# Performance work log

Measured on AMD Instinct MI355X. Metric: run time of the kernel, lower is better.

Reference implementation:

```python
import jax, jax.numpy as jnp
from jax import lax
import numpy as np


def setup_inputs() -> dict:
    key = jax.random.key(0)
    kx, kw = jax.random.split(key)
    # Binary {0,1} activations: the module's int8-cast/XOR/AND trick is only
    # meaningful XNOR-popcount math for binary inputs.
    x = jax.random.randint(kx, (32, 256, 58, 58), 0, 2).astype(jnp.float32)
    weight = jax.random.normal(kw, (256, 256, 3, 3), dtype=jnp.float32)
    return {"x": x, "weight": weight}


def reference(x, weight):
    # XNORConv2d.forward, stride=1, padding=0 (forward never pads).
    B, C, H, W = x.shape
    O, _, kh, kw = weight.shape
    n = C * H * W  # note: alpha normalizes by INPUT size, as in the source
    N = kh * kw

    # alpha = sum_{c,kh,kw} |w| / n, one scalar per output filter  -> (O,)
    alpha = jnp.sum(jnp.abs(weight), axis=(1, 2, 3)) / n

    # Binarized weights: sign(w) >= 0 -> {0,1}
    bw = (weight >= 0).astype(x.dtype)

    dn = lax.conv_dimension_numbers(x.shape, weight.shape, ("NCHW", "OIHW", "NCHW"))
    conv = lambda a, f: lax.conv_general_dilated(
        a, f, window_strides=(1, 1), padding="VALID", dimension_numbers=dn
    )

    # XNOR match count per (b, o, y, x): S = #(p==f) over c,kh,kw
    #   = conv(p, f) + conv(1-p, 1-f)
    S = conv(x, bw) + conv(1.0 - x, 1.0 - bw)  # (B, O, H', W')

    # popcount per channel = 2*s_c - N; summed over channels -> 2*S - C*N
    res = 2.0 * S - jnp.asarray(C * N, dtype=x.dtype)

    return alpha[None, :, None, None] * res
```

## Files before the change

### kernel.cpp

```cpp
#include <hip/hip_runtime.h>
#include <stdint.h>


#define BATCH 32
#define C_IN 256
#define OCH 256
#define HIN 58
#define WIN2 58
#define HOUT 56
#define WOUT 56
#define TAPS 9
#define WWORDS 8
#define HWIN (HIN * WIN2)
#define HWOUT (HOUT * WOUT)
#define NPOS (BATCH * HWIN)

#define AP 144
#define NAPOS 232

typedef int   i32x4  __attribute__((ext_vector_type(4)));
typedef int   i32x16 __attribute__((ext_vector_type(16)));
typedef float f32x4  __attribute__((ext_vector_type(4)));

#define MFMA(acc, va, vb) \
    asm volatile("v_mfma_i32_32x32x32_i8 %0, %1, %2, %0" : "+v"(acc) : "v"(va), "v"(vb))

__global__ __launch_bounds__(256) void pack_x_kernel(
    const float* __restrict__ x, uint32_t* __restrict__ xp)
{
    int t = blockIdx.x * 256 + threadIdx.x;
    int p  = t >> 2;
    int wp = t & 3;
    int b = p / HWIN;
    int r = p - b * HWIN;
    const float* xb = x + ((size_t)(b * C_IN + wp * 64)) * HWIN + r;
    uint32_t m0 = 0u, m1 = 0u;
    #pragma unroll
    for (int j = 0; j < 32; ++j) {
        float v0 = xb[(size_t)j * HWIN];
        float v1 = xb[(size_t)(j + 32) * HWIN];
        m0 |= (v0 > 0.5f ? 1u : 0u) << j;
        m1 |= (v1 > 0.5f ? 1u : 0u) << j;
    }
    *(uint2*)(xp + (size_t)p * WWORDS + wp * 2) = make_uint2(m0, m1);
}

__global__ __launch_bounds__(256) void pack_w8_kernel(
    const float* __restrict__ wt, char* __restrict__ wq8s, float* __restrict__ sA)
{
    int o = blockIdx.x;
    int c = threadIdx.x;
    const float* wb = wt + ((size_t)o * C_IN + c) * TAPS;
    float s = 0.f;
    char sg[TAPS];
    #pragma unroll
    for (int t = 0; t < TAPS; ++t) {
        float v = wb[t];
        s += fabsf(v);
        sg[t] = (v >= 0.0f) ? (char)1 : (char)-1;
    }
    int kh = c >> 7;
    int kb = (c >> 5) & 3;
    int e  = (c >> 4) & 1;
    int j  = c & 15;
    #pragma unroll
    for (int t = 0; t < TAPS; ++t) {
        int st = kh * 36 + t * 4 + kb;
        wq8s[(size_t)((st * 2 + e) * 256 + o) * 16 + j] = sg[t];
    }

    __shared__ float red[256];
    red[c] = s;
    __syncthreads();
    for (int off = 128; off > 0; off >>= 1) {
        if (c < off) red[c] += red[c + off];
        __syncthreads();
    }
    if (c == 0) sA[o] = red[0] / (float)(C_IN * HWIN);
}

__global__ __launch_bounds__(512)
void xnor_mfma_kernel(
    const uint32_t* __restrict__ xp, const char* __restrict__ wq8s,
    const float* __restrict__ sA, float* __restrict__ out)
{
    __shared__ __attribute__((aligned(16))) char lds[36864];
    char* Alds = lds;
    float* Cbuf = (float*)lds;

    int blk = blockIdx.x;
    int b   = blk / 28;
    int rp  = blk - b * 28;
    int oy0 = rp * 2;
    int tid  = threadIdx.x;
    int wv   = tid >> 6;
    int lane = tid & 63;
    int l31  = lane & 31;
    int e    = lane >> 5;
    int mgrp = wv & 1;
    int ngrp = wv >> 1;

    int baseA[2];
    #pragma unroll
    for (int mi = 0; mi < 2; ++mi) {
        int p = (mgrp * 2 + mi) * 32 + l31;
        int r = (p * 586) >> 15;
        int c = p - 56 * r;
        baseA[mi] = (r * 58 + c) * AP + e * 16;
    }
    const char* pb = wq8s + ((size_t)e * 256 + (size_t)(ngrp * 64 + l31)) * 16;
    float al0 = sA[ngrp * 64 + l31];
    float al1 = sA[ngrp * 64 + 32 + l31];

    i32x16 acc00 = {0}, acc01 = {0}, acc10 = {0}, acc11 = {0};
    asm volatile("" : "+v"(acc00), "+v"(acc01), "+v"(acc10), "+v"(acc11));
    asm volatile("s_nop 7\n\ts_nop 7");

#define STAGE_A(KH)                                                        \
    {                                                                      \
        _Pragma("unroll")                                                  \
        for (int ir = 0; ir < 4; ++ir) {                                   \
            if (tid < 464) {                                               \
                int iw = tid >> 3, c16 = tid & 7;                          \
                uint32_t wvx = xp[((size_t)(b * HIN + oy0 + ir) * WIN2 + iw) * WWORDS \
                                  + (KH) * 4 + (c16 >> 1)];                \
                uint32_t bits = (c16 & 1) ? (wvx >> 16) : (wvx & 0xFFFFu); \
                i32x4 v;                                                   \
                _Pragma("unroll")                                          \
                for (int d = 0; d < 4; ++d) {                              \
                    uint32_t n  = (bits >> (4 * d)) & 0xFu;                \
                    uint32_t sp = (n * 0x204081u) & 0x01010101u;           \
                    v[d] = (int)~(sp * 0xFEu);                             \
                }                                                          \
                *(i32x4*)(Alds + (ir * 58 + iw) * AP + c16 * 16) = v;      \
            }                                                              \
        }                                                                  \
    }

    STAGE_A(0);

    i32x4 rb0[3], rb1[3];
    #pragma unroll
    for (int q = 0; q < 3; ++q) {
        rb0[q] = *(const i32x4*)(pb + (size_t)q * 8192);
        rb1[q] = *(const i32x4*)(pb + (size_t)q * 8192 + 512);
    }
    __syncthreads();

    #pragma unroll
    for (int s = 0; s < 72; ++s) {
        if (s == 36) {
            __syncthreads();
            STAGE_A(1);
            __syncthreads();
        }
        const int kh  = s / 36;
        const int tap = (s - kh * 36) >> 2;
        const int kb  = s & 3;
        const int dy  = tap / 3, dx = tap - dy * 3;
        const int ka  = (dy * 58 + dx) * AP + kb * 32;

        i32x4 a0 = *(const i32x4*)(Alds + baseA[0] + ka);
        i32x4 a1 = *(const i32x4*)(Alds + baseA[1] + ka);
        i32x4 b0 = rb0[s % 3];
        i32x4 b1 = rb1[s % 3];
        MFMA(acc00, a0, b0);
        MFMA(acc01, a0, b1);
        MFMA(acc10, a1, b0);
        MFMA(acc11, a1, b1);

        const int s3 = (s + 3 > 71) ? 71 : s + 3;
        rb0[s % 3] = *(const i32x4*)(pb + (size_t)s3 * 8192);
        rb1[s % 3] = *(const i32x4*)(pb + (size_t)s3 * 8192 + 512);
    }

    asm volatile("s_nop 7\n\ts_nop 7");

    size_t ob = ((size_t)b * OCH) * HWOUT + (size_t)oy0 * WOUT;
    #pragma unroll
    for (int q = 0; q < 4; ++q) {
        __syncthreads();
        if (mgrp == (q >> 1)) {
            const int mi = q & 1;
            #pragma unroll
            for (int ni = 0; ni < 2; ++ni) {
                float al = ni ? al1 : al0;
                int o = ngrp * 64 + ni * 32 + l31;
                i32x16 A;
                if (mi == 0 && ni == 0) A = acc00;
                else if (mi == 0)       A = acc01;
                else if (ni == 0)       A = acc10;
                else                    A = acc11;
                #pragma unroll
                for (int g = 0; g < 4; ++g) {
                    f32x4 vv;
                    vv[0] = al * (float)A[4 * g + 0];
                    vv[1] = al * (float)A[4 * g + 1];
                    vv[2] = al * (float)A[4 * g + 2];
                    vv[3] = al * (float)A[4 * g + 3];
                    int pl = g * 8 + 4 * e;
                    *(f32x4*)(Cbuf + (size_t)o * 36 + pl) = vv;
                }
            }
        }
        __syncthreads();
        #pragma unroll 1
        for (int i = 0; i < 16; ++i) {
            int idx = i * 512 + tid;
            int o = idx >> 5, pl = idx & 31;
            int pg = q * 32 + pl;
            if (pg < 112) {
                int r = (pg >= 56) ? 1 : 0;
                int c = pg - 56 * r;
                out[ob + (size_t)o * HWOUT + r * WOUT + c] = Cbuf[o * 36 + pl];
            }
        }
    }
#undef STAGE_A
}

extern "C" void kernel_launch(void* const* d_in, const int* in_sizes, int n_in,
                              void* d_out, int out_size, void* d_ws, size_t ws_size,
                              hipStream_t stream)
{
    const float* x  = (const float*)d_in[0];
    const float* wt = (const float*)d_in[1];
    float* out = (float*)d_out;

    char* ws = (char*)d_ws;
    uint32_t* xp   = (uint32_t*)ws;
    char*     wq8s = (char*)(ws + 3444736);
    float*    sAp  = (float*)(ws + 3444736 + 589824);

    pack_x_kernel<<<dim3(1682), dim3(256), 0, stream>>>(x, xp);

    pack_w8_kernel<<<dim3(OCH), dim3(256), 0, stream>>>(wt, wq8s, sAp);

    xnor_mfma_kernel<<<dim3(896), dim3(512), 0, stream>>>(xp, wq8s, sAp, out);
}
```

Measured before the change: 268.9 us.

## Prefetch LDS A fragments, move accumulators to AGPRs, repack x per position

```diff
diff --git a/kernel.cpp b/kernel.cpp
--- a/kernel.cpp
+++ b/kernel.cpp
@@ -23,26 +23,27 @@
 typedef float f32x4  __attribute__((ext_vector_type(4)));
 
 #define MFMA(acc, va, vb) \
-    asm volatile("v_mfma_i32_32x32x32_i8 %0, %1, %2, %0" : "+v"(acc) : "v"(va), "v"(vb))
+    asm volatile("v_mfma_i32_32x32x32_i8 %0, %1, %2, %0" : "+a"(acc) : "v"(va), "v"(vb))
 
 __global__ __launch_bounds__(256) void pack_x_kernel(
     const float* __restrict__ x, uint32_t* __restrict__ xp)
 {
-    int t = blockIdx.x * 256 + threadIdx.x;
-    int p  = t >> 2;
-    int wp = t & 3;
+    int p = blockIdx.x * 256 + threadIdx.x;
+    if (p >= NPOS) return;
     int b = p / HWIN;
     int r = p - b * HWIN;
-    const float* xb = x + ((size_t)(b * C_IN + wp * 64)) * HWIN + r;
-    uint32_t m0 = 0u, m1 = 0u;
-    #pragma unroll
-    for (int j = 0; j < 32; ++j) {
-        float v0 = xb[(size_t)j * HWIN];
-        float v1 = xb[(size_t)(j + 32) * HWIN];
-        m0 |= (v0 > 0.5f ? 1u : 0u) << j;
-        m1 |= (v1 > 0.5f ? 1u : 0u) << j;
-    }
-    *(uint2*)(xp + (size_t)p * WWORDS + wp * 2) = make_uint2(m0, m1);
+    const float* xb = x + (size_t)b * C_IN * HWIN + r;
+    uint32_t w[8];
+    #pragma unroll
+    for (int k = 0; k < 8; ++k) {
+        uint32_t m = 0u;
+        #pragma unroll
+        for (int j = 0; j < 32; ++j)
+            m |= (xb[(size_t)(k * 32 + j) * HWIN] > 0.5f ? 1u : 0u) << j;
+        w[k] = m;
+    }
+    *(uint4*)(xp + (size_t)p * WWORDS)     = make_uint4(w[0], w[1], w[2], w[3]);
+    *(uint4*)(xp + (size_t)p * WWORDS + 4) = make_uint4(w[4], w[5], w[6], w[7]);
 }
 
 __global__ __launch_bounds__(256) void pack_w8_kernel(
@@ -80,6 +81,7 @@
 }
 
 __global__ __launch_bounds__(512)
+__attribute__((amdgpu_waves_per_eu(4)))
 void xnor_mfma_kernel(
     const uint32_t* __restrict__ xp, const char* __restrict__ wq8s,
     const float* __restrict__ sA, float* __restrict__ out)
@@ -113,8 +115,10 @@
     float al1 = sA[ngrp * 64 + 32 + l31];
 
     i32x16 acc00 = {0}, acc01 = {0}, acc10 = {0}, acc11 = {0};
-    asm volatile("" : "+v"(acc00), "+v"(acc01), "+v"(acc10), "+v"(acc11));
+    asm volatile("" : "+a"(acc00), "+a"(acc01), "+a"(acc10), "+a"(acc11));
     asm volatile("s_nop 7\n\ts_nop 7");
+
+#define KA(s) ((((((s) % 36) >> 2) / 3) * 58 + ((((s) % 36) >> 2) % 3)) * AP + ((s) & 3) * 32)
 
 #define STAGE_A(KH)                                                        \
     {                                                                      \
@@ -147,31 +151,34 @@
     }
     __syncthreads();
 
+    i32x4 a0c = *(const i32x4*)(Alds + baseA[0] + KA(0));
+    i32x4 a1c = *(const i32x4*)(Alds + baseA[1] + KA(0));
+
     #pragma unroll
     for (int s = 0; s < 72; ++s) {
         if (s == 36) {
             __syncthreads();
             STAGE_A(1);
             __syncthreads();
+            a0c = *(const i32x4*)(Alds + baseA[0] + KA(36));
+            a1c = *(const i32x4*)(Alds + baseA[1] + KA(36));
         }
-        const int kh  = s / 36;
-        const int tap = (s - kh * 36) >> 2;
-        const int kb  = s & 3;
-        const int dy  = tap / 3, dx = tap - dy * 3;
-        const int ka  = (dy * 58 + dx) * AP + kb * 32;
-
-        i32x4 a0 = *(const i32x4*)(Alds + baseA[0] + ka);
-        i32x4 a1 = *(const i32x4*)(Alds + baseA[1] + ka);
+        const int s3 = (s + 3 > 71) ? 71 : s + 3;
+        i32x4 nb0 = *(const i32x4*)(pb + (size_t)s3 * 8192);
+        i32x4 nb1 = *(const i32x4*)(pb + (size_t)s3 * 8192 + 512);
+        const int sn = (s == 35 || s == 71) ? s : s + 1;
+        i32x4 na0 = *(const i32x4*)(Alds + baseA[0] + KA(sn));
+        i32x4 na1 = *(const i32x4*)(Alds + baseA[1] + KA(sn));
+
         i32x4 b0 = rb0[s % 3];
         i32x4 b1 = rb1[s % 3];
-        MFMA(acc00, a0, b0);
-        MFMA(acc01, a0, b1);
-        MFMA(acc10, a1, b0);
-        MFMA(acc11, a1, b1);
-
-        const int s3 = (s + 3 > 71) ? 71 : s + 3;
-        rb0[s % 3] = *(const i32x4*)(pb + (size_t)s3 * 8192);
-        rb1[s % 3] = *(const i32x4*)(pb + (size_t)s3 * 8192 + 512);
+        MFMA(acc00, a0c, b0);
+        MFMA(acc01, a0c, b1);
+        MFMA(acc10, a1c, b0);
+        MFMA(acc11, a1c, b1);
+
+        rb0[s % 3] = nb0; rb1[s % 3] = nb1;
+        a0c = na0; a1c = na1;
     }
 
     asm volatile("s_nop 7\n\ts_nop 7");
@@ -217,6 +224,7 @@
         }
     }
 #undef STAGE_A
+#undef KA
 }
 
 extern "C" void kernel_launch(void* const* d_in, const int* in_sizes, int n_in,
@@ -232,7 +240,7 @@
     char*     wq8s = (char*)(ws + 3444736);
     float*    sAp  = (float*)(ws + 3444736 + 589824);
 
-    pack_x_kernel<<<dim3(1682), dim3(256), 0, stream>>>(x, xp);
+    pack_x_kernel<<<dim3((NPOS + 255) / 256), dim3(256), 0, stream>>>(x, xp);
 
     pack_w8_kernel<<<dim3(OCH), dim3(256), 0, stream>>>(wt, wq8s, sAp);
 
```

Result: slower. 301.9 us (+12.3%).
